# Performance work log

Measured on AMD Instinct MI355X. Metric: run time of the kernel, lower is better.

## Reference

```python
import jax, jax.numpy as jnp
import numpy as np

SIZE = (2, 2)

def setup_inputs() -> dict:
    key = jax.random.key(0)
    k1, k2 = jax.random.split(key)
    B, H, W, C = 16, 128, 128, 64
    OH, OW = H * SIZE[0], W * SIZE[1]
    updates = jax.random.normal(k1, (B, H, W, C), dtype=jnp.float32)
    argmax = jax.random.randint(k2, (B, H, W, C), 0, OH * OW * C, dtype=jnp.int32)
    return {"updates": updates, "argmax": argmax}

def reference(updates, argmax):
    # Max-unpooling: scatter pooled values into an upsampled map at argmax positions.
    B, H, W, C = updates.shape
    OH, OW = H * SIZE[0], W * SIZE[1]
    # Decode flattened argmax (TF convention: ((y*OW + x)*C + c)) -> (y, x).
    y = (argmax // (OW * C)) % OH            # [B,H,W,C]
    x = (argmax // C) % OW                   # [B,H,W,C]
    # Batch and channel indices come from position, matching the TF code
    # (channel is taken from a tiled arange, NOT argmax % C).
    b = jnp.arange(B, dtype=jnp.int32).reshape(B, 1, 1, 1)
    c = jnp.arange(C, dtype=jnp.int32).reshape(1, 1, 1, C)
    out = jnp.zeros((B, OH, OW, C), dtype=updates.dtype)
    # tf.scatter_nd sums duplicate indices -> use .add
    out = out.at[b, y, x, c].add(updates)
    return out
```

## Files before the change

### kernel.cpp

```cpp
#include <hip/hip_runtime.h>


#define C_      64
#define N_ELEM  (16 * 128 * 128 * 64)
#define NB      1024
#define ST      512
#define CHE     8192
#define NBIN    512
#define NGB     8192
#define REGION  8192
#define PADCAP  (CHE + NBIN)

__device__ __forceinline__ unsigned int f2bf(float f) {
    unsigned int u = __float_as_uint(f);
    return (u + 0x7fffu + ((u >> 16) & 1u)) >> 16;
}

__global__ __launch_bounds__(ST) void scatter_sort_kernel(
        const float4* __restrict__ upd4, const int4* __restrict__ amx4,
        unsigned int* __restrict__ pairs, int* __restrict__ lofs) {
    __shared__ unsigned int staging[PADCAP];
    __shared__ int h[NBIN];
    __shared__ int wsc[17];

    int t = threadIdx.x, lane = t & 63, w = t >> 6;
    int blk = blockIdx.x;
    int cc = (t & 15) << 2;

    int base4 = blk * 4096;
    int4 a[4]; float4 u[4];
    #pragma unroll
    for (int q = 0; q < 4; ++q) {
        a[q] = amx4[base4 + q * ST + t];
        u[q] = upd4[base4 + q * ST + t];
    }

    #pragma unroll
    for (int ch = 0; ch < 2; ++ch) {
        int bins[16]; unsigned int prs[16];
        #pragma unroll
        for (int q = 0; q < 4; ++q) {
            bins[4*q+0] = (a[q].x >> 13) & 511;
            prs [4*q+0] = (((unsigned)(a[q].x & 0x1FC0) | cc)       << 16) | f2bf(u[q].x);
            bins[4*q+1] = (a[q].y >> 13) & 511;
            prs [4*q+1] = (((unsigned)(a[q].y & 0x1FC0) | (cc + 1)) << 16) | f2bf(u[q].y);
            bins[4*q+2] = (a[q].z >> 13) & 511;
            prs [4*q+2] = (((unsigned)(a[q].z & 0x1FC0) | (cc + 2)) << 16) | f2bf(u[q].z);
            bins[4*q+3] = (a[q].w >> 13) & 511;
            prs [4*q+3] = (((unsigned)(a[q].w & 0x1FC0) | (cc + 3)) << 16) | f2bf(u[q].w);
        }
        if (ch == 0) {
            #pragma unroll
            for (int q = 0; q < 4; ++q) {
                a[q] = amx4[base4 + 2048 + q * ST + t];
                u[q] = upd4[base4 + 2048 + q * ST + t];
            }
        }

        h[t] = 0;
        __syncthreads();
        #pragma unroll
        for (int j = 0; j < 16; ++j) atomicAdd(&h[bins[j]], 1);
        __syncthreads();

        int cnt = h[t];
        int pcnt = (cnt + 1) & ~1;
        int incl = pcnt;
        #pragma unroll
        for (int off = 1; off < 64; off <<= 1) {
            int nv = __shfl_up(incl, off, 64);
            if (lane >= off) incl += nv;
        }
        if (lane == 63) wsc[w] = incl;
        __syncthreads();
        if (t < 8) {
            int s = 0;
            for (int j = 0; j < t; ++j) s += wsc[j];
            wsc[8 + t] = s;
        }
        __syncthreads();
        int excl = incl - pcnt + wsc[8 + w];
        h[t] = excl;
        int row = (2 * blk + ch) * 513;
        lofs[row + t] = excl;
        if (t == 511) {
            lofs[row + 512] = excl + pcnt;
            wsc[16] = excl + pcnt;
        }
        __syncthreads();

        if (cnt & 1) staging[excl + cnt] = 0u;
        #pragma unroll
        for (int j = 0; j < 16; ++j) {
            int slot = atomicAdd(&h[bins[j]], 1);
            staging[slot] = prs[j];
        }
        __syncthreads();

        int padM = wsc[16];
        uint4* dst = (uint4*)(pairs + (size_t)(2 * blk + ch) * PADCAP);
        int n4v = (padM + 3) >> 2;
        for (int k = t; k < n4v; k += ST)
            dst[k] = make_uint4(staging[4*k], staging[4*k+1],
                                staging[4*k+2], staging[4*k+3]);
        __syncthreads();
    }
}

__global__ __launch_bounds__(ST) void gather_accum_kernel(
        const unsigned int* __restrict__ pairs, const int* __restrict__ lofs,
        float4* __restrict__ out4) {
    __shared__ float acc[REGION];
    int g = blockIdx.x, t = threadIdx.x;
    int b = g >> 9, bin = g & 511;

    int seg = t >> 2, l4 = t & 3;
    int row = (b * 128 + seg) * 513 + bin;
    int s = lofs[row];
    int e = lofs[row + 1];
    int cnt2 = (e - s) >> 1;
    const uint2* base2 = (const uint2*)pairs
        + (((size_t)(b * 128 + seg) * PADCAP + s) >> 1);

    #pragma unroll
    for (int q = 0; q < 4; ++q)
        *(float4*)&acc[(q * ST + t) * 4] = make_float4(0.f, 0.f, 0.f, 0.f);
    __syncthreads();

    for (int i = l4; i < cnt2; i += 4) {
        uint2 p = base2[i];
        atomicAdd(&acc[p.x >> 16], __uint_as_float(p.x << 16));
        atomicAdd(&acc[p.y >> 16], __uint_as_float(p.y << 16));
    }
    __syncthreads();

    float4* dst = out4 + (size_t)g * (REGION / 4);
    #pragma unroll
    for (int q = 0; q < 4; ++q) {
        int k = q * ST + t;
        dst[k] = make_float4(acc[4*k], acc[4*k+1], acc[4*k+2], acc[4*k+3]);
    }
}

__global__ void zero_out_kernel(float4* __restrict__ out, int n4) {
    int stride = gridDim.x * blockDim.x;
    for (int i = blockIdx.x * blockDim.x + threadIdx.x; i < n4; i += stride)
        out[i] = make_float4(0.f, 0.f, 0.f, 0.f);
}

__global__ void unpool_atomic_kernel(const float4* __restrict__ upd4,
                                     const int4* __restrict__ amx4,
                                     float* __restrict__ out, int n4) {
    int i = blockIdx.x * blockDim.x + threadIdx.x;
    if (i >= n4) return;
    float4 u = upd4[i];
    int4   a = amx4[i];
    int e = i << 2;
    int c = e & (C_ - 1);
    int base_b = (e >> 20) << 22;
    int y, x;
    y = (a.x >> 14) & 255; x = (a.x >> 6) & 255;
    atomicAdd(&out[base_b + (y << 14) + (x << 6) + c], u.x);
    y = (a.y >> 14) & 255; x = (a.y >> 6) & 255;
    atomicAdd(&out[base_b + (y << 14) + (x << 6) + c + 1], u.y);
    y = (a.z >> 14) & 255; x = (a.z >> 6) & 255;
    atomicAdd(&out[base_b + (y << 14) + (x << 6) + c + 2], u.z);
    y = (a.w >> 14) & 255; x = (a.w >> 6) & 255;
    atomicAdd(&out[base_b + (y << 14) + (x << 6) + c + 3], u.w);
}

extern "C" void kernel_launch(void* const* d_in, const int* in_sizes, int n_in,
                              void* d_out, int out_size, void* d_ws, size_t ws_size,
                              hipStream_t stream) {
    const float* updates = (const float*)d_in[0];
    const int*   argmax  = (const int*)d_in[1];

    size_t pair_bytes = (size_t)NB * 2 * PADCAP * 4;
    size_t lofs_bytes = (size_t)NB * 2 * 513 * 4;
    size_t need = pair_bytes + lofs_bytes;

    if (in_sizes[0] == N_ELEM && ws_size >= need) {
        char* ws = (char*)d_ws;
        unsigned int* pairs = (unsigned int*)ws;
        int*          lofs  = (int*)(ws + pair_bytes);

        scatter_sort_kernel<<<NB, ST, 0, stream>>>(
            (const float4*)updates, (const int4*)argmax, pairs, lofs);
        gather_accum_kernel<<<NGB, ST, 0, stream>>>(pairs, lofs, (float4*)d_out);
    } else {
        int n_out4 = out_size >> 2;
        zero_out_kernel<<<2048, 256, 0, stream>>>((float4*)d_out, n_out4);
        int n4 = in_sizes[0] >> 2;
        unpool_atomic_kernel<<<(n4 + 255) / 256, 256, 0, stream>>>(
            (const float4*)updates, (const int4*)argmax, (float*)d_out, n4);
    }
}
```

Baseline: 154.4 us.

## Balance gather work across wavefront lanes via segment prefix-sum and binary search

In the gather kernel, each wavefront now owns 16 segments, computes an exclusive prefix sum of their pair counts with shuffles, and spreads the combined pair list evenly across all 64 lanes. Each lane finds its segment with a shuffle-based binary search. Before, 4 lanes per segment looped over that segment's own count, so lanes sat idle when counts differed. The change adds shuffle overhead per iteration, and the loads are no longer contiguous within a segment's lane group.

```diff
diff --git a/kernel.cpp b/kernel.cpp
--- a/kernel.cpp
+++ b/kernel.cpp
@@ -113,24 +113,49 @@
     __shared__ float acc[REGION];
     int g = blockIdx.x, t = threadIdx.x;
     int b = g >> 9, bin = g & 511;
-
-    int seg = t >> 2, l4 = t & 3;
+    int lane = t & 63, w = t >> 6;
+
+    int seg = w * 16 + (lane & 15);
     int row = (b * 128 + seg) * 513 + bin;
-    int s = lofs[row];
-    int e = lofs[row + 1];
-    int cnt2 = (e - s) >> 1;
-    const uint2* base2 = (const uint2*)pairs
-        + (((size_t)(b * 128 + seg) * PADCAP + s) >> 1);
+    int s = 0, cnt2 = 0;
+    if (lane < 16) {
+        s = lofs[row];
+        cnt2 = (lofs[row + 1] - s) >> 1;
+    }
+    int segS2 = s >> 1;
+
+    int incl = cnt2;
+    #pragma unroll
+    for (int off = 1; off < 16; off <<= 1) {
+        int nv = __shfl_up(incl, off, 64);
+        if (lane >= off && lane < 16) incl += nv;
+    }
+    int runB = incl - cnt2;
+    int M2 = __shfl(incl, 15, 64);
 
     #pragma unroll
     for (int q = 0; q < 4; ++q)
         *(float4*)&acc[(q * ST + t) * 4] = make_float4(0.f, 0.f, 0.f, 0.f);
     __syncthreads();
 
-    for (int i = l4; i < cnt2; i += 4) {
-        uint2 p = base2[i];
-        atomicAdd(&acc[p.x >> 16], __uint_as_float(p.x << 16));
-        atomicAdd(&acc[p.y >> 16], __uint_as_float(p.y << 16));
+    const uint2* pr2 = (const uint2*)pairs;
+    size_t wbase2 = ((size_t)(b * 128 + w * 16) * PADCAP) >> 1;
+    for (int m2base = 0; m2base < M2; m2base += 64) {
+        int m2 = m2base + lane;
+        int lo = 0;
+        #pragma unroll
+        for (int stp = 8; stp; stp >>= 1) {
+            int cand = lo + stp;
+            int rb = __shfl(runB, cand, 64);
+            if (cand < 16 && rb <= m2) lo = cand;
+        }
+        int rbLo = __shfl(runB, lo, 64);
+        int ssLo = __shfl(segS2, lo, 64);
+        if (m2 < M2) {
+            uint2 p = pr2[wbase2 + (size_t)lo * (PADCAP / 2) + ssLo + (m2 - rbLo)];
+            atomicAdd(&acc[p.x >> 16], __uint_as_float(p.x << 16));
+            atomicAdd(&acc[p.y >> 16], __uint_as_float(p.y << 16));
+        }
     }
     __syncthreads();
 
```

After: 169.2 us. +9.5%, slower.
